# Kernel tuning notes

Hardware: AMD Instinct MI355X
Metric: run time of the kernel (lower is better)

Reference implementation:

```python
import jax, jax.numpy as jnp
import numpy as np

N_QUBITS = 4
N_LAYERS = 2
BATCH = 524288


def _ry(theta):
    # RY(theta) = [[cos(t/2), -sin(t/2)], [sin(t/2), cos(t/2)]], shape [..., 2, 2]
    c = jnp.cos(theta / 2)
    s = jnp.sin(theta / 2)
    return jnp.stack([jnp.stack([c, -s], -1), jnp.stack([s, c], -1)], -2).astype(jnp.complex64)


def _rz(theta):
    # RZ(theta) = diag(exp(-i t/2), exp(i t/2))
    p = jnp.exp(-1j * theta / 2)
    pc = jnp.exp(1j * theta / 2)
    z = jnp.zeros_like(p)
    return jnp.stack([jnp.stack([p, z], -1), jnp.stack([z, pc], -1)], -2).astype(jnp.complex64)


def _apply_1q(state, gate, q):
    # state: [B,2,2,2,2] (axis 1+q is qubit q, wire 0 most significant as in default.qubit)
    # gate: [2,2] (shared) or [B,2,2] (per-sample)
    letters = list('abcd')
    t = letters[q]
    out = letters.copy()
    out[q] = 'z'
    if gate.ndim == 3:
        sub = f"Bz{t},B{''.join(letters)}->B{''.join(out)}"
    else:
        sub = f"z{t},B{''.join(letters)}->B{''.join(out)}"
    return jnp.einsum(sub, gate, state)


def _cnot(state, c, t):
    # flip target axis on the control=1 slice
    s0 = jnp.take(state, 0, axis=1 + c)
    s1 = jnp.take(state, 1, axis=1 + c)
    ta = 1 + t - (1 if t > c else 0)
    s1 = jnp.flip(s1, axis=ta)
    return jnp.stack([s0, s1], axis=1 + c)


def _circuit(x, weights):
    B = x.shape[0]
    state = jnp.zeros((B, 2, 2, 2, 2), jnp.complex64).at[:, 0, 0, 0, 0].set(1.0)
    ry_in = _ry(x)  # [B, 4, 2, 2], per-sample input encoding
    for q in range(N_QUBITS):
        state = _apply_1q(state, ry_in[:, q], q)
    for l in range(N_LAYERS):
        for q in range(N_QUBITS):
            state = _apply_1q(state, _rz(weights[l, q, 0]), q)
            state = _apply_1q(state, _ry(weights[l, q, 1]), q)
        for q in range(N_QUBITS - 1):
            state = _cnot(state, q, q + 1)
        state = _cnot(state, N_QUBITS - 1, 0)
    probs = jnp.abs(state.reshape(B, 16)) ** 2
    # <Z_i> = sum_s p(s) * (1 - 2*bit_i(s)); wire 0 is the most significant bit
    bits = (np.arange(16)[:, None] >> np.arange(N_QUBITS - 1, -1, -1)) & 1
    signs = jnp.asarray(1.0 - 2.0 * bits, jnp.float32)  # [16, 4]
    return probs @ signs  # [B, 4]


def setup_inputs() -> dict:
    key = jax.random.key(0)
    k1, k2 = jax.random.split(key)
    x = jax.random.normal(k1, (BATCH, N_QUBITS), dtype=jnp.float32)
    # TorchLayer default init: uniform in [0, 2*pi)
    weights = jax.random.uniform(k2, (N_LAYERS, N_QUBITS, 2), dtype=jnp.float32, minval=0.0, maxval=2 * np.pi)
    return {"x": x, "weights": weights}


def reference(x, weights):
    return _circuit(x, weights)
```

## Files before the change

kernel.cpp:

```cpp
#include <hip/hip_runtime.h>

#define BATCH 524288
#define TPB 256
#define V 2

__global__ void qprep_kernel(const float* __restrict__ w, float* __restrict__ ws) {
    const int tid = threadIdx.x;
    if (tid >= 16) return;

    float stx[16], sty[16];
    #pragma unroll
    for (int i = 0; i < 16; i++) { stx[i] = 0.f; sty[i] = 0.f; }
    stx[tid] = 1.f;

    #pragma unroll
    for (int l = 0; l < 2; l++) {
        #pragma unroll
        for (int q = 0; q < 4; q++) {
            float cz, sz, cy, sy;
            __sincosf(0.5f * w[l * 8 + q * 2 + 0], &sz, &cz);
            __sincosf(0.5f * w[l * 8 + q * 2 + 1], &sy, &cy);
            const int mask = 8 >> q;
            #pragma unroll
            for (int i = 0; i < 16; i++) {
                float ax = stx[i], ay = sty[i];
                if (i & mask) { stx[i] = ax * cz - ay * sz; sty[i] = ay * cz + ax * sz; }
                else          { stx[i] = ax * cz + ay * sz; sty[i] = ay * cz - ax * sz; }
            }
            #pragma unroll
            for (int i = 0; i < 16; i++) {
                if (!(i & mask)) {
                    float a0x = stx[i], a0y = sty[i];
                    float a1x = stx[i | mask], a1y = sty[i | mask];
                    stx[i]        = cy * a0x - sy * a1x;
                    sty[i]        = cy * a0y - sy * a1y;
                    stx[i | mask] = sy * a0x + cy * a1x;
                    sty[i | mask] = sy * a0y + cy * a1y;
                }
            }
        }
        #pragma unroll
        for (int e = 0; e < 4; e++) {
            const int cqs[4] = {0, 1, 2, 3};
            const int tqs[4] = {1, 2, 3, 0};
            const int cm = 8 >> cqs[e];
            const int tm = 8 >> tqs[e];
            #pragma unroll
            for (int i = 0; i < 16; i++) {
                if ((i & cm) && !(i & tm)) {
                    float t0x = stx[i], t0y = sty[i];
                    stx[i] = stx[i | tm]; sty[i] = sty[i | tm];
                    stx[i | tm] = t0x;    sty[i | tm] = t0y;
                }
            }
        }
    }
    #pragma unroll
    for (int j = 0; j < 16; j++) {
        ws[j * 32 + tid]      = stx[j];
        ws[j * 32 + 16 + tid] = sty[j];
    }
}

__global__ __launch_bounds__(TPB, 4) void qmain_kernel(const float* __restrict__ x,
                                                       const float* __restrict__ U,
                                                       float* __restrict__ out) {
    const int base = blockIdx.x * (TPB * V) + threadIdx.x;

    float sv[V][16];
    #pragma unroll
    for (int v = 0; v < V; v++) {
        const int smp = base + v * TPB;
        const float4 xv = reinterpret_cast<const float4*>(x)[smp];
        float c0, s0, c1, s1, c2, s2, c3, s3;
        __sincosf(0.5f * xv.x, &s0, &c0);
        __sincosf(0.5f * xv.y, &s1, &c1);
        __sincosf(0.5f * xv.z, &s2, &c2);
        __sincosf(0.5f * xv.w, &s3, &c3);
        const float p01[4] = {c0 * c1, c0 * s1, s0 * c1, s0 * s1};
        const float p23[4] = {c2 * c3, c2 * s3, s2 * c3, s2 * s3};
        #pragma unroll
        for (int i = 0; i < 16; i++) sv[v][i] = p01[i >> 2] * p23[i & 3];
    }

    float z[V][4];
    #pragma unroll
    for (int v = 0; v < V; v++)
        #pragma unroll
        for (int i = 0; i < 4; i++) z[v][i] = 0.f;

    #pragma unroll
    for (int j = 0; j < 16; j++) {
        float re[V], im[V];
        #pragma unroll
        for (int v = 0; v < V; v++) { re[v] = 0.f; im[v] = 0.f; }
        #pragma unroll
        for (int k = 0; k < 16; k++) {
            const float ur = U[j * 32 + k];
            const float ui = U[j * 32 + 16 + k];
            #pragma unroll
            for (int v = 0; v < V; v++) {
                re[v] = fmaf(ur, sv[v][k], re[v]);
                im[v] = fmaf(ui, sv[v][k], im[v]);
            }
        }
        #pragma unroll
        for (int v = 0; v < V; v++) {
            const float p = re[v] * re[v] + im[v] * im[v];
            z[v][0] += (j & 8) ? -p : p;
            z[v][1] += (j & 4) ? -p : p;
            z[v][2] += (j & 2) ? -p : p;
            z[v][3] += (j & 1) ? -p : p;
        }
    }

    #pragma unroll
    for (int v = 0; v < V; v++) {
        const int smp = base + v * TPB;
        reinterpret_cast<float4*>(out)[smp] = make_float4(z[v][0], z[v][1], z[v][2], z[v][3]);
    }
}

extern "C" void kernel_launch(void* const* d_in, const int* in_sizes, int n_in,
                              void* d_out, int out_size, void* d_ws, size_t ws_size,
                              hipStream_t stream) {
    const float* x = (const float*)d_in[0];
    const float* w = (const float*)d_in[1];
    float* out = (float*)d_out;
    float* U = (float*)d_ws;

    qprep_kernel<<<1, 64, 0, stream>>>(w, U);
    const int grid = BATCH / (TPB * V);
    qmain_kernel<<<grid, TPB, 0, stream>>>(x, U, out);
}
```

Measured before the change: 69.24 us.

## Use one sample per thread with inline-asm scalar loads of the unitary

```diff
diff --git a/kernel.cpp b/kernel.cpp
--- a/kernel.cpp
+++ b/kernel.cpp
@@ -2,7 +2,8 @@
 
 #define BATCH 524288
 #define TPB 256
-#define V 2
+
+typedef float vfloat16 __attribute__((ext_vector_type(16)));
 
 __global__ void qprep_kernel(const float* __restrict__ w, float* __restrict__ ws) {
     const int tid = threadIdx.x;
@@ -17,9 +18,10 @@
     for (int l = 0; l < 2; l++) {
         #pragma unroll
         for (int q = 0; q < 4; q++) {
-            float cz, sz, cy, sy;
-            __sincosf(0.5f * w[l * 8 + q * 2 + 0], &sz, &cz);
-            __sincosf(0.5f * w[l * 8 + q * 2 + 1], &sy, &cy);
+            const float tz = 0.5f * w[l * 8 + q * 2 + 0];
+            const float ty = 0.5f * w[l * 8 + q * 2 + 1];
+            const float cz = __cosf(tz), sz = __sinf(tz);
+            const float cy = __cosf(ty), sy = __sinf(ty);
             const int mask = 8 >> q;
             #pragma unroll
             for (int i = 0; i < 16; i++) {
@@ -62,63 +64,48 @@
     }
 }
 
-__global__ __launch_bounds__(TPB, 4) void qmain_kernel(const float* __restrict__ x,
+__global__ __launch_bounds__(TPB, 8) void qmain_kernel(const float* __restrict__ x,
                                                        const float* __restrict__ U,
                                                        float* __restrict__ out) {
-    const int base = blockIdx.x * (TPB * V) + threadIdx.x;
+    const int base = blockIdx.x * TPB + threadIdx.x;
 
-    float sv[V][16];
+    const float4 xv = reinterpret_cast<const float4*>(x)[base];
+    const float h0 = 0.5f * xv.x, h1 = 0.5f * xv.y, h2 = 0.5f * xv.z, h3 = 0.5f * xv.w;
+    const float c0 = __cosf(h0), s0 = __sinf(h0);
+    const float c1 = __cosf(h1), s1 = __sinf(h1);
+    const float c2 = __cosf(h2), s2 = __sinf(h2);
+    const float c3 = __cosf(h3), s3 = __sinf(h3);
+
+    const float p01[4] = {c0 * c1, c0 * s1, s0 * c1, s0 * s1};
+    const float p23[4] = {c2 * c3, c2 * s3, s2 * c3, s2 * s3};
+    float sv[16];
     #pragma unroll
-    for (int v = 0; v < V; v++) {
-        const int smp = base + v * TPB;
-        const float4 xv = reinterpret_cast<const float4*>(x)[smp];
-        float c0, s0, c1, s1, c2, s2, c3, s3;
-        __sincosf(0.5f * xv.x, &s0, &c0);
-        __sincosf(0.5f * xv.y, &s1, &c1);
-        __sincosf(0.5f * xv.z, &s2, &c2);
-        __sincosf(0.5f * xv.w, &s3, &c3);
-        const float p01[4] = {c0 * c1, c0 * s1, s0 * c1, s0 * s1};
-        const float p23[4] = {c2 * c3, c2 * s3, s2 * c3, s2 * s3};
-        #pragma unroll
-        for (int i = 0; i < 16; i++) sv[v][i] = p01[i >> 2] * p23[i & 3];
-    }
+    for (int i = 0; i < 16; i++) sv[i] = p01[i >> 2] * p23[i & 3];
 
-    float z[V][4];
-    #pragma unroll
-    for (int v = 0; v < V; v++)
-        #pragma unroll
-        for (int i = 0; i < 4; i++) z[v][i] = 0.f;
+    float z0 = 0.f, z1 = 0.f, z2 = 0.f, z3 = 0.f;
 
     #pragma unroll
     for (int j = 0; j < 16; j++) {
-        float re[V], im[V];
-        #pragma unroll
-        for (int v = 0; v < V; v++) { re[v] = 0.f; im[v] = 0.f; }
+        vfloat16 ur, ui;
+        asm volatile("s_load_dwordx16 %0, %2, 0x0\n\t"
+                     "s_load_dwordx16 %1, %2, 0x40\n\t"
+                     "s_waitcnt lgkmcnt(0)"
+                     : "=s"(ur), "=s"(ui)
+                     : "s"(U + j * 32));
+        float re = 0.f, im = 0.f;
         #pragma unroll
         for (int k = 0; k < 16; k++) {
-            const float ur = U[j * 32 + k];
-            const float ui = U[j * 32 + 16 + k];
-            #pragma unroll
-            for (int v = 0; v < V; v++) {
-                re[v] = fmaf(ur, sv[v][k], re[v]);
-                im[v] = fmaf(ui, sv[v][k], im[v]);
-            }
+            re = fmaf(ur[k], sv[k], re);
+            im = fmaf(ui[k], sv[k], im);
         }
-        #pragma unroll
-        for (int v = 0; v < V; v++) {
-            const float p = re[v] * re[v] + im[v] * im[v];
-            z[v][0] += (j & 8) ? -p : p;
-            z[v][1] += (j & 4) ? -p : p;
-            z[v][2] += (j & 2) ? -p : p;
-            z[v][3] += (j & 1) ? -p : p;
-        }
+        const float p = re * re + im * im;
+        z0 += (j & 8) ? -p : p;
+        z1 += (j & 4) ? -p : p;
+        z2 += (j & 2) ? -p : p;
+        z3 += (j & 1) ? -p : p;
     }
 
-    #pragma unroll
-    for (int v = 0; v < V; v++) {
-        const int smp = base + v * TPB;
-        reinterpret_cast<float4*>(out)[smp] = make_float4(z[v][0], z[v][1], z[v][2], z[v][3]);
-    }
+    reinterpret_cast<float4*>(out)[base] = make_float4(z0, z1, z2, z3);
 }
 
 extern "C" void kernel_launch(void* const* d_in, const int* in_sizes, int n_in,
@@ -130,6 +117,5 @@
     float* U = (float*)d_ws;
 
     qprep_kernel<<<1, 64, 0, stream>>>(w, U);
-    const int grid = BATCH / (TPB * V);
-    qmain_kernel<<<grid, TPB, 0, stream>>>(x, U, out);
+    qmain_kernel<<<BATCH / TPB, TPB, 0, stream>>>(x, U, out);
 }
```

Measured after the change: 71.79 us. 1.04x slower.
